# Optimization experiments

Hardware: AMD Instinct MI355X
Metric: run time of the kernel (lower is better)

Reference implementation:

```python
import jax, jax.numpy as jnp
import numpy as np

NUM_GROUPS = 16
FEAT_DIM = 512
BATCH = 32768


def setup_inputs() -> dict:
    key = jax.random.key(0)
    k1, k2 = jax.random.split(key)
    group_feats = jax.random.normal(k1, (NUM_GROUPS, BATCH, FEAT_DIM), dtype=jnp.float32)
    centers = jax.random.normal(k2, (NUM_GROUPS, FEAT_DIM), dtype=jnp.float32)
    return {"group_feats": group_feats, "centers": centers}


def reference(group_feats, centers):
    # group_feats: (G, B, D) -> per-sample (B, G, D)
    gf = jnp.transpose(group_feats, (1, 0, 2))  # (B, G, D)
    # F.normalize(centers): row-wise L2 normalize with eps=1e-12
    norm = jnp.sqrt(jnp.sum(centers * centers, axis=1, keepdims=True))
    c = centers / jnp.maximum(norm, 1e-12)  # (G, D)
    # Original builds a (G,G) distmat per sample then masks with eye, so only
    # the diagonal survives: d_i = ||g_i||^2 + ||c_i||^2 - 2 g_i . c_i
    g_sq = jnp.sum(gf * gf, axis=-1)                 # (B, G)
    c_sq = jnp.sum(c * c, axis=-1)                   # (G,)
    cross = jnp.einsum('bgd,gd->bg', gf, c)          # (B, G)
    diag = g_sq + c_sq[None, :] - 2.0 * cross        # (B, G)
    per_sample = jnp.sum(jnp.clip(diag, 1e-12, 1e12), axis=1) / NUM_GROUPS  # (B,)
    loss = jnp.mean(per_sample)
    return loss
```

## Files before the change

### kernel.cpp

```cpp
#include <hip/hip_runtime.h>
#include <math.h>

#define NG 16
#define NB 32768
#define ND 512

__global__ void normalize_centers_kernel(const float* __restrict__ centers,
                                         float* __restrict__ cnorm) {
    const int g = blockIdx.x;
    const int t = threadIdx.x;
    const float2 v = *reinterpret_cast<const float2*>(centers + g * ND + t * 2);
    float ss = v.x * v.x + v.y * v.y;

    #pragma unroll
    for (int off = 1; off < 64; off <<= 1)
        ss += __shfl_xor(ss, off, 64);

    __shared__ float wsum[4];
    const int lane = t & 63;
    const int wave = t >> 6;
    if (lane == 0) wsum[wave] = ss;
    __syncthreads();
    const float tot = wsum[0] + wsum[1] + wsum[2] + wsum[3];
    const float inv = 1.0f / fmaxf(sqrtf(tot), 1e-12f);

    float2 o;
    o.x = v.x * inv;
    o.y = v.y * inv;
    *reinterpret_cast<float2*>(cnorm + g * ND + t * 2) = o;
}

__global__ __launch_bounds__(256) void compact_loss_kernel(
        const float* __restrict__ gf,
        const float* __restrict__ cnorm,
        float* __restrict__ out) {
    const int g    = blockIdx.y;
    const int lane = threadIdx.x & 63;
    const int wave = threadIdx.x >> 6;

    const float4 c0 = *reinterpret_cast<const float4*>(cnorm + g * ND + lane * 4);
    const float4 c1 = *reinterpret_cast<const float4*>(cnorm + g * ND + 256 + lane * 4);

    const float* base = gf + (size_t)g * NB * ND;
    const int waves_per_g = gridDim.x * 4;
    const int wid = blockIdx.x * 4 + wave;

    float acc = 0.0f;
    for (int b = wid; b < NB; b += waves_per_g) {
        const float* row = base + (size_t)b * ND;
        const float4 v0 = *reinterpret_cast<const float4*>(row + lane * 4);
        const float4 v1 = *reinterpret_cast<const float4*>(row + 256 + lane * 4);

        float d, s;
        d = v0.x - c0.x; s  = d * d;
        d = v0.y - c0.y; s += d * d;
        d = v0.z - c0.z; s += d * d;
        d = v0.w - c0.w; s += d * d;
        d = v1.x - c1.x; s += d * d;
        d = v1.y - c1.y; s += d * d;
        d = v1.z - c1.z; s += d * d;
        d = v1.w - c1.w; s += d * d;

        #pragma unroll
        for (int off = 1; off < 64; off <<= 1)
            s += __shfl_xor(s, off, 64);

        s = fminf(fmaxf(s, 1e-12f), 1e12f);
        acc += s;
    }

    __shared__ float wacc[4];
    if (lane == 0) wacc[wave] = acc;
    __syncthreads();
    if (threadIdx.x == 0) {
        const float tot = (wacc[0] + wacc[1] + wacc[2] + wacc[3])
                          * (1.0f / ((float)NG * (float)NB));
        atomicAdd(out, tot);
    }
}

extern "C" void kernel_launch(void* const* d_in, const int* in_sizes, int n_in,
                              void* d_out, int out_size, void* d_ws, size_t ws_size,
                              hipStream_t stream) {
    const float* gf      = (const float*)d_in[0];
    const float* centers = (const float*)d_in[1];
    float* out           = (float*)d_out;
    float* cnorm         = (float*)d_ws;

    hipMemsetAsync(out, 0, sizeof(float) * out_size, stream);

    normalize_centers_kernel<<<dim3(NG), dim3(256), 0, stream>>>(centers, cnorm);

    compact_loss_kernel<<<dim3(128, NG), dim3(256), 0, stream>>>(gf, cnorm, out);
}
```

Measured before the change: 197.6 us.

## Fuse center normalization into loss kernel, unroll rows by two, use nontemporal loads

Folds the center-normalization kernel into the main loss kernel, so each block recomputes its group's center norm and skips a separate launch and the workspace round trip. The main loop now processes two rows per wave per iteration, putting more loads in flight, and it reads the streaming input with nontemporal loads to avoid polluting the cache. In exchange, each of the many blocks repeats the small norm reduction and an extra barrier, and register use grows. The two-row stride assumes the row count divides evenly, which holds for the fixed sizes.

Result: faster. 172.7 us (-12.6%).

```diff
diff --git a/kernel.cpp b/kernel.cpp
--- a/kernel.cpp
+++ b/kernel.cpp
@@ -5,77 +5,83 @@
 #define NB 32768
 #define ND 512
 
-__global__ void normalize_centers_kernel(const float* __restrict__ centers,
-                                         float* __restrict__ cnorm) {
-    const int g = blockIdx.x;
-    const int t = threadIdx.x;
-    const float2 v = *reinterpret_cast<const float2*>(centers + g * ND + t * 2);
-    float ss = v.x * v.x + v.y * v.y;
+typedef float f32x4 __attribute__((ext_vector_type(4)));
 
+__global__ __launch_bounds__(256) void compact_loss_kernel(
+        const float* __restrict__ gf,
+        const float* __restrict__ centers,
+        float* __restrict__ out) {
+    const int g    = blockIdx.y;
+    const int t    = threadIdx.x;
+    const int lane = t & 63;
+    const int wave = t >> 6;
+
+    const float2 cv = *reinterpret_cast<const float2*>(centers + g * ND + t * 2);
+    float ss = cv.x * cv.x + cv.y * cv.y;
     #pragma unroll
     for (int off = 1; off < 64; off <<= 1)
         ss += __shfl_xor(ss, off, 64);
-
     __shared__ float wsum[4];
-    const int lane = t & 63;
-    const int wave = t >> 6;
     if (lane == 0) wsum[wave] = ss;
     __syncthreads();
     const float tot = wsum[0] + wsum[1] + wsum[2] + wsum[3];
     const float inv = 1.0f / fmaxf(sqrtf(tot), 1e-12f);
 
-    float2 o;
-    o.x = v.x * inv;
-    o.y = v.y * inv;
-    *reinterpret_cast<float2*>(cnorm + g * ND + t * 2) = o;
-}
-
-__global__ __launch_bounds__(256) void compact_loss_kernel(
-        const float* __restrict__ gf,
-        const float* __restrict__ cnorm,
-        float* __restrict__ out) {
-    const int g    = blockIdx.y;
-    const int lane = threadIdx.x & 63;
-    const int wave = threadIdx.x >> 6;
-
-    const float4 c0 = *reinterpret_cast<const float4*>(cnorm + g * ND + lane * 4);
-    const float4 c1 = *reinterpret_cast<const float4*>(cnorm + g * ND + 256 + lane * 4);
+    f32x4 c0 = *reinterpret_cast<const f32x4*>(centers + g * ND + lane * 4);
+    f32x4 c1 = *reinterpret_cast<const f32x4*>(centers + g * ND + 256 + lane * 4);
+    c0 *= inv;
+    c1 *= inv;
 
     const float* base = gf + (size_t)g * NB * ND;
     const int waves_per_g = gridDim.x * 4;
     const int wid = blockIdx.x * 4 + wave;
 
     float acc = 0.0f;
-    for (int b = wid; b < NB; b += waves_per_g) {
-        const float* row = base + (size_t)b * ND;
-        const float4 v0 = *reinterpret_cast<const float4*>(row + lane * 4);
-        const float4 v1 = *reinterpret_cast<const float4*>(row + 256 + lane * 4);
+    for (int b = wid; b < NB; b += 2 * waves_per_g) {
+        const float* rowA = base + (size_t)b * ND;
+        const float* rowB = base + (size_t)(b + waves_per_g) * ND;
+        const f32x4 a0 = __builtin_nontemporal_load(reinterpret_cast<const f32x4*>(rowA + lane * 4));
+        const f32x4 a1 = __builtin_nontemporal_load(reinterpret_cast<const f32x4*>(rowA + 256 + lane * 4));
+        const f32x4 b0 = __builtin_nontemporal_load(reinterpret_cast<const f32x4*>(rowB + lane * 4));
+        const f32x4 b1 = __builtin_nontemporal_load(reinterpret_cast<const f32x4*>(rowB + 256 + lane * 4));
 
-        float d, s;
-        d = v0.x - c0.x; s  = d * d;
-        d = v0.y - c0.y; s += d * d;
-        d = v0.z - c0.z; s += d * d;
-        d = v0.w - c0.w; s += d * d;
-        d = v1.x - c1.x; s += d * d;
-        d = v1.y - c1.y; s += d * d;
-        d = v1.z - c1.z; s += d * d;
-        d = v1.w - c1.w; s += d * d;
+        float d, sA, sB;
+        d = a0.x - c0.x; sA  = d * d;
+        d = a0.y - c0.y; sA += d * d;
+        d = a0.z - c0.z; sA += d * d;
+        d = a0.w - c0.w; sA += d * d;
+        d = a1.x - c1.x; sA += d * d;
+        d = a1.y - c1.y; sA += d * d;
+        d = a1.z - c1.z; sA += d * d;
+        d = a1.w - c1.w; sA += d * d;
+
+        d = b0.x - c0.x; sB  = d * d;
+        d = b0.y - c0.y; sB += d * d;
+        d = b0.z - c0.z; sB += d * d;
+        d = b0.w - c0.w; sB += d * d;
+        d = b1.x - c1.x; sB += d * d;
+        d = b1.y - c1.y; sB += d * d;
+        d = b1.z - c1.z; sB += d * d;
+        d = b1.w - c1.w; sB += d * d;
 
         #pragma unroll
-        for (int off = 1; off < 64; off <<= 1)
-            s += __shfl_xor(s, off, 64);
+        for (int off = 1; off < 64; off <<= 1) {
+            sA += __shfl_xor(sA, off, 64);
+            sB += __shfl_xor(sB, off, 64);
+        }
 
-        s = fminf(fmaxf(s, 1e-12f), 1e12f);
-        acc += s;
+        sA = fminf(fmaxf(sA, 1e-12f), 1e12f);
+        sB = fminf(fmaxf(sB, 1e-12f), 1e12f);
+        acc += sA + sB;
     }
 
     __shared__ float wacc[4];
     if (lane == 0) wacc[wave] = acc;
     __syncthreads();
-    if (threadIdx.x == 0) {
-        const float tot = (wacc[0] + wacc[1] + wacc[2] + wacc[3])
-                          * (1.0f / ((float)NG * (float)NB));
-        atomicAdd(out, tot);
+    if (t == 0) {
+        const float totb = (wacc[0] + wacc[1] + wacc[2] + wacc[3])
+                           * (1.0f / ((float)NG * (float)NB));
+        atomicAdd(out, totb);
     }
 }
 
@@ -85,11 +91,8 @@
     const float* gf      = (const float*)d_in[0];
     const float* centers = (const float*)d_in[1];
     float* out           = (float*)d_out;
-    float* cnorm         = (float*)d_ws;
 
     hipMemsetAsync(out, 0, sizeof(float) * out_size, stream);
 
-    normalize_centers_kernel<<<dim3(NG), dim3(256), 0, stream>>>(centers, cnorm);
-
-    compact_loss_kernel<<<dim3(128, NG), dim3(256), 0, stream>>>(gf, cnorm, out);
+    compact_loss_kernel<<<dim3(128, NG), dim3(256), 0, stream>>>(gf, centers, out);
 }
```
